# Kernel optimization log

Hardware: AMD Instinct MI355X
Metric: run time of the kernel (lower is better)

Reference implementation:

```python
import jax, jax.numpy as jnp
import numpy as np

N_NODES = 10000
N_EDGES = 160000
N_GRAPHS = 64
F = 80        # hidden dim
T = 5         # towers
F_OUT = 16    # per-tower post output (80/5)
N_LAYERS = 4
EPS = 1e-6
BN_EPS = 1e-5
STD_EPS = 1e-5


def setup_inputs() -> dict:
    key = jax.random.key(0)
    ks = jax.random.split(key, 12)
    x = jax.random.uniform(ks[0], (N_NODES, 2), dtype=jnp.float32)
    edge_index = jax.random.randint(ks[1], (2, N_EDGES), 0, N_NODES, dtype=jnp.int64)
    batch = jnp.sort(jax.random.randint(ks[2], (N_NODES,), 0, N_GRAPHS, dtype=jnp.int64))

    def w(k, shape, fan_in):
        return (jax.random.normal(k, shape, jnp.float32) / np.float32(np.sqrt(fan_in)))

    return {
        "x": x, "edge_index": edge_index, "batch": batch,
        "pre_lin_W": w(ks[3], (1, F), 1), "pre_lin_b": jnp.zeros((F,), jnp.float32),
        "pre_W": w(ks[4], (N_LAYERS, T, 2 * F, F), 2 * F), "pre_b": jnp.zeros((N_LAYERS, T, F), jnp.float32),
        "post_W": w(ks[5], (N_LAYERS, T, 13 * F, F_OUT), 13 * F), "post_b": jnp.zeros((N_LAYERS, T, F_OUT), jnp.float32),
        "lin_W": w(ks[6], (N_LAYERS, F, F), F), "lin_b": jnp.zeros((N_LAYERS, F), jnp.float32),
        "bn_gamma": jnp.ones((N_LAYERS, F), jnp.float32), "bn_beta": jnp.zeros((N_LAYERS, F), jnp.float32),
        "mlp_lin_W": w(ks[7], (40, 1), 40), "mlp_lin_b": jnp.zeros((1,), jnp.float32),
        "mlp1_W": w(ks[8], (40, 20), 40), "mlp1_b": jnp.zeros((20,), jnp.float32),
        "mlp2_W": w(ks[9], (20, 1), 20), "mlp2_b": jnp.zeros((1,), jnp.float32),
    }


def _pna_conv(h, src, dst, deg, avg_log_deg, preW, preb, postW, postb, linW, linb):
    # h: [N, F]; messages per tower: pre MLP over cat(x_i, x_j)  (divide_input=False)
    N = h.shape[0]
    hm = jnp.concatenate([h[dst], h[src]], axis=-1)            # [E, 2F]
    m = jnp.einsum('ef,tfo->eto', hm, preW) + preb             # [E, T, F]

    cnt = jnp.maximum(deg, 1.0)[:, None, None]                 # [N,1,1]
    has = (deg > 0)[:, None, None]
    s = jax.ops.segment_sum(m, dst, num_segments=N)
    mean = s / cnt
    mean_sq = jax.ops.segment_sum(m * m, dst, num_segments=N) / cnt
    mn = jax.ops.segment_min(m, dst, num_segments=N)
    mx = jax.ops.segment_max(m, dst, num_segments=N)
    mn = jnp.where(has, mn, 0.0)
    mx = jnp.where(has, mx, 0.0)
    std = jnp.sqrt(jax.nn.relu(mean_sq - mean * mean) + STD_EPS)
    agg = jnp.concatenate([mean, mn, mx, std], axis=-1)        # [N, T, 4F]

    logd = jnp.log(jnp.maximum(deg, 1.0) + 1.0)[:, None, None]
    amp = agg * (logd / avg_log_deg)
    att = agg * (avg_log_deg / logd)
    out = jnp.concatenate([agg, amp, att], axis=-1)            # [N, T, 12F]

    xt = jnp.broadcast_to(h[:, None, :], (N, T, F))
    out = jnp.concatenate([xt, out], axis=-1)                  # [N, T, 13F]
    out = jnp.einsum('ntf,tfo->nto', out, postW) + postb       # [N, T, F_OUT]
    out = out.reshape(N, T * F_OUT)                            # [N, 80]
    return out @ linW + linb


def _forward(x, edge_index, batch, pre_lin_W, pre_lin_b, pre_W, pre_b,
             post_W, post_b, lin_W, lin_b, bn_gamma, bn_beta,
             mlp_lin_W, mlp_lin_b, mlp1_W, mlp1_b, mlp2_W, mlp2_b):
    N = x.shape[0]
    src, dst = edge_index[0], edge_index[1]
    deg = jax.ops.segment_sum(jnp.ones_like(dst, jnp.float32), dst, num_segments=N)
    avg_log_deg = jnp.mean(jnp.log(deg + 1.0))                 # PNA avg log-degree from deg histogram

    operation = x[:, 0:1]
    assignment = x[:, 1:2]
    op = operation @ pre_lin_W + pre_lin_b                     # [N, 80]

    for l in range(N_LAYERS):
        y = _pna_conv(op, src, dst, deg, avg_log_deg,
                      pre_W[l], pre_b[l], post_W[l], post_b[l], lin_W[l], lin_b[l])
        mu = jnp.mean(y, axis=0)
        var = jnp.mean((y - mu) ** 2, axis=0)                  # biased, training-mode BN
        y = (y - mu) / jnp.sqrt(var + BN_EPS) * bn_gamma[l] + bn_beta[l]
        op = jax.nn.relu(y)

    front, behind = op[:, :40], op[:, 40:]
    xc = front * assignment + behind                           # [N, 40], non-negative

    # LastLayer: log-space scatter-add message passing
    log_score = jax.ops.segment_sum(jnp.log(xc[src] + EPS), dst, num_segments=N)
    xc = jnp.exp(log_score + jnp.log(xc + EPS))

    # global mean pool over graphs
    gcnt = jnp.maximum(jax.ops.segment_sum(jnp.ones_like(batch, jnp.float32), batch, num_segments=N_GRAPHS), 1.0)
    pooled = jax.ops.segment_sum(xc, batch, num_segments=N_GRAPHS) / gcnt[:, None]  # [B, 40]

    x_lin = pooled @ mlp_lin_W + mlp_lin_b
    x_cv = pooled @ mlp1_W + mlp1_b
    x_cv = 20.0 - jax.nn.relu(x_cv)
    x_cv = x_cv @ mlp2_W + mlp2_b
    return x_cv + x_lin                                        # [B, 1]


def reference(x, edge_index, batch, pre_lin_W, pre_lin_b, pre_W, pre_b,
              post_W, post_b, lin_W, lin_b, bn_gamma, bn_beta,
              mlp_lin_W, mlp_lin_b, mlp1_W, mlp1_b, mlp2_W, mlp2_b):
    return _forward(x, edge_index, batch, pre_lin_W, pre_lin_b, pre_W, pre_b,
                    post_W, post_b, lin_W, lin_b, bn_gamma, bn_beta,
                    mlp_lin_W, mlp_lin_b, mlp1_W, mlp1_b, mlp2_W, mlp2_b)
```

## Files before the change

kernel.cpp:

```cpp
#include <hip/hip_runtime.h>
#include <math.h>

#define NN 10000
#define NE 160000
#define NG 64
#define FEAT 80
#define NT 5
#define NL 4

__global__ void k_count(const int* __restrict__ dst, int* __restrict__ deg) {
    int e = blockIdx.x * 256 + threadIdx.x;
    if (e < NE) atomicAdd(&deg[dst[e]], 1);
}

__global__ void k_gcnt(const int* __restrict__ batch, int* __restrict__ gcnt) {
    int n = blockIdx.x * 256 + threadIdx.x;
    if (n < NN) atomicAdd(&gcnt[batch[n]], 1);
}

__global__ void k_scan(const int* __restrict__ deg, int* __restrict__ offs) {
    __shared__ int sums[256];
    int tid = threadIdx.x;
    int start = tid * 40, stop = min(start + 40, NN);
    int s = 0;
    for (int i = start; i < stop; ++i) s += deg[i];
    sums[tid] = s;
    __syncthreads();
    for (int off = 1; off < 256; off <<= 1) {
        int v = (tid >= off) ? sums[tid - off] : 0;
        __syncthreads();
        sums[tid] += v;
        __syncthreads();
    }
    int base = (tid == 0) ? 0 : sums[tid - 1];
    for (int i = start; i < stop; ++i) { offs[i] = base; base += deg[i]; }
    if (tid == 255) offs[NN] = sums[255];
}

__global__ void k_ald(const int* __restrict__ deg, float* __restrict__ ald) {
    __shared__ float red[256];
    int i = blockIdx.x * 256 + threadIdx.x;
    red[threadIdx.x] = (i < NN) ? logf((float)deg[i] + 1.0f) : 0.0f;
    __syncthreads();
    for (int s = 128; s > 0; s >>= 1) {
        if (threadIdx.x < s) red[threadIdx.x] += red[threadIdx.x + s];
        __syncthreads();
    }
    if (threadIdx.x == 0) atomicAdd(ald, red[0]);
}

__global__ void k_fill(const int* __restrict__ src, const int* __restrict__ dst,
                       const int* __restrict__ offs, int* __restrict__ cursor,
                       int* __restrict__ csr) {
    int e = blockIdx.x * 256 + threadIdx.x;
    if (e < NE) {
        int d = dst[e];
        int p = atomicAdd(&cursor[d], 1);
        csr[offs[d] + p] = src[e];
    }
}

__global__ void k_op0(const float* __restrict__ x, const float* __restrict__ plW,
                      const float* __restrict__ plb, float* __restrict__ hT) {
    int i = blockIdx.x * 256 + threadIdx.x;
    if (i < FEAT * NN) {
        int f = i / NN, n = i - f * NN;
        hT[i] = x[2 * n] * plW[f] + plb[f];
    }
}

__global__ __launch_bounds__(256) void k_mm_ab(
        const float* __restrict__ hT, const float* __restrict__ preW_l,
        float* __restrict__ A, float* __restrict__ Bt) {
    __shared__ float hs[16][80];
    int n0 = blockIdx.x * 16;
    int tid = threadIdx.x;
    for (int i = tid; i < 16 * 80; i += 256) {
        int nl = i & 15, f = i >> 4;
        hs[nl][f] = hT[(size_t)f * NN + n0 + nl];
    }
    __syncthreads();
    int c0 = blockIdx.y * 512 + tid;
    float acc[2][16];
#pragma unroll
    for (int s = 0; s < 2; s++)
#pragma unroll
        for (int i = 0; i < 16; i++) acc[s][i] = 0.f;
    const float* wp[2];
#pragma unroll
    for (int s = 0; s < 2; s++) {
        int c = c0 + s * 256;
        int part = (c >= 400) ? 1 : 0;
        int cc = c - part * 400;
        int t = cc / 80, o = cc - t * 80;
        wp[s] = preW_l + (size_t)(t * 160 + part * 80) * 80 + o;
    }
    bool act1 = (c0 + 256) < 800;
    for (int fq = 0; fq < 80; fq += 4) {
        float w0a = wp[0][(fq + 0) * 80], w0b = wp[0][(fq + 1) * 80];
        float w0c = wp[0][(fq + 2) * 80], w0d = wp[0][(fq + 3) * 80];
        float w1a = 0.f, w1b = 0.f, w1c = 0.f, w1d = 0.f;
        if (act1) {
            w1a = wp[1][(fq + 0) * 80]; w1b = wp[1][(fq + 1) * 80];
            w1c = wp[1][(fq + 2) * 80]; w1d = wp[1][(fq + 3) * 80];
        }
#pragma unroll
        for (int i = 0; i < 16; i++) {
            float4 hv = *(const float4*)&hs[i][fq];
            acc[0][i] += hv.x * w0a + hv.y * w0b + hv.z * w0c + hv.w * w0d;
            acc[1][i] += hv.x * w1a + hv.y * w1b + hv.z * w1c + hv.w * w1d;
        }
    }
#pragma unroll
    for (int s = 0; s < 2; s++) {
        int c = c0 + s * 256;
        if (c < 800) {
            int part = (c >= 400) ? 1 : 0;
            int cc = c - part * 400;
            int t = cc / 80, o = cc - t * 80;
            if (part == 0) {
#pragma unroll
                for (int i = 0; i < 16; i++) A[(size_t)(n0 + i) * 400 + cc] = acc[s][i];
            } else {
#pragma unroll
                for (int i = 0; i < 16; i++)
                    Bt[((size_t)t * NN + n0 + i) * 80 + o] = acc[s][i];
            }
        }
    }
}

__global__ __launch_bounds__(256) void k_agg_t(
        const float* __restrict__ A, const float* __restrict__ Bt,
        const int* __restrict__ offs, const int* __restrict__ csr,
        const float* __restrict__ preb_l, float* __restrict__ aggT) {
    __shared__ float st[320 * 17];
    int tid = threadIdx.x;
    int t = blockIdx.y;
    int n0 = blockIdx.x * 16;
    int ni = tid >> 4;
    int cl = tid & 15;
    int n = n0 + ni;
    int e0 = offs[n], e1 = offs[n + 1];
    const float* Bts = Bt + (size_t)t * NN * 80;
    float s[5], q[5], mn[5], mx[5];
#pragma unroll
    for (int k = 0; k < 5; k++) { s[k] = 0.f; q[k] = 0.f; mn[k] = 3.4e38f; mx[k] = -3.4e38f; }
    int e = e0;
    for (; e + 3 < e1; e += 4) {
        const float* br0 = Bts + (size_t)csr[e] * 80 + cl;
        const float* br1 = Bts + (size_t)csr[e + 1] * 80 + cl;
        const float* br2 = Bts + (size_t)csr[e + 2] * 80 + cl;
        const float* br3 = Bts + (size_t)csr[e + 3] * 80 + cl;
#pragma unroll
        for (int k = 0; k < 5; k++) {
            float b0 = br0[k * 16];
            float b1 = br1[k * 16];
            float b2 = br2[k * 16];
            float b3 = br3[k * 16];
            s[k] += (b0 + b1) + (b2 + b3);
            q[k] += (b0 * b0 + b1 * b1) + (b2 * b2 + b3 * b3);
            mn[k] = fminf(mn[k], fminf(fminf(b0, b1), fminf(b2, b3)));
            mx[k] = fmaxf(mx[k], fmaxf(fmaxf(b0, b1), fmaxf(b2, b3)));
        }
    }
    for (; e < e1; ++e) {
        const float* br = Bts + (size_t)csr[e] * 80 + cl;
#pragma unroll
        for (int k = 0; k < 5; k++) {
            float b = br[k * 16];
            s[k] += b; q[k] += b * b;
            mn[k] = fminf(mn[k], b); mx[k] = fmaxf(mx[k], b);
        }
    }
    int d = e1 - e0;
    float degf = (float)d;
    float cnt = fmaxf(degf, 1.f);
#pragma unroll
    for (int k = 0; k < 5; k++) {
        int c = cl + k * 16;
        float a = A[(size_t)n * 400 + t * 80 + c] + preb_l[t * 80 + c];
        float mean = (degf * a + s[k]) / cnt;
        float msq  = (degf * a * a + 2.f * a * s[k] + q[k]) / cnt;
        float sd = sqrtf(fmaxf(msq - mean * mean, 0.f) + 1e-5f);
        float mnr = (d > 0) ? a + mn[k] : 0.f;
        float mxr = (d > 0) ? a + mx[k] : 0.f;
        st[(0 * 80 + c) * 17 + ni] = mean;
        st[(1 * 80 + c) * 17 + ni] = mnr;
        st[(2 * 80 + c) * 17 + ni] = mxr;
        st[(3 * 80 + c) * 17 + ni] = sd;
    }
    __syncthreads();
    int jj = tid >> 4;
    int nl = tid & 15;
#pragma unroll
    for (int pass = 0; pass < 20; ++pass) {
        int j = pass * 16 + jj;
        aggT[((size_t)t * 320 + j) * NN + n0 + nl] = st[j * 17 + nl];
    }
}

__global__ __launch_bounds__(256) void k_post(
        const float* __restrict__ hT, const float* __restrict__ aggT,
        const float* __restrict__ postW_l, const float* __restrict__ postb_l,
        const int* __restrict__ offs, const float* __restrict__ ald_sum,
        float* __restrict__ y0T) {
    __shared__ float wj[80 * 48];
    __shared__ float wh[80 * 16];
    int tid = threadIdx.x;
    int t = blockIdx.y;
    int jq = blockIdx.z;
    int j0 = jq * 80;
    const float* W0 = postW_l + (size_t)t * 1040 * 16;
    const float* W1 = W0 + 80 * 16;
    const float* W2 = W0 + 400 * 16;
    const float* W3 = W0 + 720 * 16;
    for (int idx = tid; idx < 80 * 48; idx += 256) {
        int j = idx / 48;
        int rem = idx - j * 48;
        int p = rem >> 4, o = rem & 15;
        const float* Wp = (p == 0) ? W1 : (p == 1) ? W2 : W3;
        wj[idx] = Wp[(j0 + j) * 16 + o];
    }
    if (jq == 0) {
        for (int idx = tid; idx < 80 * 16; idx += 256)
            wh[idx] = W0[idx];
    }
    __syncthreads();
    int n = blockIdx.x * 256 + tid;
    bool alive = (n < NN);
    int nc = alive ? n : 0;
    float acc1[16], acc2[16], acc3[16];
#pragma unroll
    for (int i = 0; i < 16; i++) { acc1[i] = 0.f; acc2[i] = 0.f; acc3[i] = 0.f; }
    const float* ap = aggT + ((size_t)t * 320 + j0) * NN + nc;
#pragma unroll 8
    for (int j = 0; j < 80; ++j) {
        float a = ap[(size_t)j * NN];
        const float* w = wj + j * 48;
#pragma unroll
        for (int i = 0; i < 16; i++) {
            acc1[i] += a * w[i];
            acc2[i] += a * w[16 + i];
            acc3[i] += a * w[32 + i];
        }
    }
    if (jq == 0) {
#pragma unroll 4
        for (int f = 0; f < 80; ++f) {
            float hv = hT[(size_t)f * NN + nc];
            const float* w = wh + f * 16;
#pragma unroll
            for (int i = 0; i < 16; i++) acc1[i] += hv * w[i];
        }
    }
    if (alive) {
        float degf = (float)(offs[n + 1] - offs[n]);
        float ald = ald_sum[0] * (1.f / NN);
        float logd = logf(fmaxf(degf, 1.f) + 1.f);
        float c1 = logd / ald;
        float c2 = ald / logd;
#pragma unroll
        for (int i = 0; i < 16; i++) {
            float v = acc1[i] + c1 * acc2[i] + c2 * acc3[i];
            if (jq == 0) v += postb_l[t * 16 + i];
            unsafeAtomicAdd(&y0T[(size_t)(t * 16 + i) * NN + n], v);
        }
    }
}

__global__ __launch_bounds__(256) void k_lin(
        const float* __restrict__ y0T, const float* __restrict__ linW_l,
        const float* __restrict__ linb_l, float* __restrict__ yT) {
    __shared__ float ws[80 * 8];
    int tid = threadIdx.x;
    int f0 = blockIdx.y * 8;
    for (int idx = tid; idx < 80 * 8; idx += 256)
        ws[idx] = linW_l[(idx >> 3) * 80 + f0 + (idx & 7)];
    __syncthreads();
    int n = blockIdx.x * 256 + tid;
    bool alive = (n < NN);
    int nc = alive ? n : 0;
    float acc[8];
#pragma unroll
    for (int i = 0; i < 8; i++) acc[i] = 0.f;
#pragma unroll 8
    for (int k = 0; k < 80; ++k) {
        float v = y0T[(size_t)k * NN + nc];
        const float4 wa = *(const float4*)(ws + k * 8);
        const float4 wb = *(const float4*)(ws + k * 8 + 4);
        acc[0] += v * wa.x; acc[1] += v * wa.y; acc[2] += v * wa.z; acc[3] += v * wa.w;
        acc[4] += v * wb.x; acc[5] += v * wb.y; acc[6] += v * wb.z; acc[7] += v * wb.w;
    }
    if (alive) {
#pragma unroll
        for (int i = 0; i < 8; i++)
            yT[(size_t)(f0 + i) * NN + n] = acc[i] + linb_l[f0 + i];
    }
}

__global__ void k_bnstats(const float* __restrict__ yT, float* __restrict__ bnst) {
    __shared__ float r1[256], r2[256];
    int f = blockIdx.x;
    int tid = threadIdx.x;
    float s = 0.f, q = 0.f;
    for (int i = tid; i < NN; i += 256) {
        float v = yT[(size_t)f * NN + i];
        s += v; q += v * v;
    }
    r1[tid] = s; r2[tid] = q;
    __syncthreads();
    for (int st = 128; st > 0; st >>= 1) {
        if (tid < st) { r1[tid] += r1[tid + st]; r2[tid] += r2[tid + st]; }
        __syncthreads();
    }
    if (tid == 0) { bnst[f] = r1[0]; bnst[80 + f] = r2[0]; }
}

__global__ void k_bn(const float* __restrict__ yT, const float* __restrict__ bnst,
                     const float* __restrict__ gamma_l, const float* __restrict__ beta_l,
                     float* __restrict__ hT) {
    int i = blockIdx.x * 256 + threadIdx.x;
    if (i >= FEAT * NN) return;
    int f = i / NN;
    float mu = bnst[f] * (1.f / NN);
    float msq = bnst[80 + f] * (1.f / NN);
    float var = fmaxf(msq - mu * mu, 0.f);
    float v = (yT[i] - mu) * (1.f / sqrtf(var + 1e-5f)) * gamma_l[f] + beta_l[f];
    hT[i] = fmaxf(v, 0.f);
}

__global__ void k_xc(const float* __restrict__ hT, const float* __restrict__ x,
                     float* __restrict__ lxc) {
    int i = blockIdx.x * 256 + threadIdx.x;
    if (i >= 40 * NN) return;
    int j = i / NN, n = i - j * NN;
    float v = hT[(size_t)j * NN + n] * x[2 * n + 1] + hT[(size_t)(40 + j) * NN + n];
    lxc[(size_t)n * 40 + j] = logf(v + 1e-6f);
}

__global__ void k_logagg(const float* __restrict__ lxc, const int* __restrict__ offs,
                         const int* __restrict__ csr, const int* __restrict__ batch,
                         float* __restrict__ pooled) {
    int n = blockIdx.x;
    int tid = threadIdx.x;
    if (tid >= 40) return;
    int e0 = offs[n], e1 = offs[n + 1];
    float s = 0.f;
    for (int k = e0; k < e1; ++k) s += lxc[(size_t)csr[k] * 40 + tid];
    float v = expf(s + lxc[(size_t)n * 40 + tid]);
    atomicAdd(&pooled[batch[n] * 40 + tid], v);
}

__global__ void k_final(const float* __restrict__ pooled, const int* __restrict__ gcnt,
                        const float* __restrict__ mlW, const float* __restrict__ mlb,
                        const float* __restrict__ m1W, const float* __restrict__ m1b,
                        const float* __restrict__ m2W, const float* __restrict__ m2b,
                        float* __restrict__ out) {
    int g = threadIdx.x;
    if (g >= NG) return;
    float inv = 1.f / fmaxf((float)gcnt[g], 1.f);
    float pl[40];
#pragma unroll
    for (int j = 0; j < 40; j++) pl[j] = pooled[g * 40 + j] * inv;
    float xl = mlb[0];
#pragma unroll
    for (int j = 0; j < 40; j++) xl += pl[j] * mlW[j];
    float acc = m2b[0];
    for (int k = 0; k < 20; k++) {
        float v = m1b[k];
#pragma unroll
        for (int j = 0; j < 40; j++) v += pl[j] * m1W[j * 20 + k];
        v = 20.f - fmaxf(v, 0.f);
        acc += v * m2W[k];
    }
    out[g] = acc + xl;
}

extern "C" void kernel_launch(void* const* d_in, const int* in_sizes, int n_in,
                              void* d_out, int out_size, void* d_ws, size_t ws_size,
                              hipStream_t stream) {
    const float* x     = (const float*)d_in[0];
    const int*   ei    = (const int*)d_in[1];
    const int*   batch = (const int*)d_in[2];
    const float* plW   = (const float*)d_in[3];
    const float* plb   = (const float*)d_in[4];
    const float* preW  = (const float*)d_in[5];
    const float* preb  = (const float*)d_in[6];
    const float* postW = (const float*)d_in[7];
    const float* postb = (const float*)d_in[8];
    const float* linW  = (const float*)d_in[9];
    const float* linb  = (const float*)d_in[10];
    const float* bnG   = (const float*)d_in[11];
    const float* bnB   = (const float*)d_in[12];
    const float* mlW   = (const float*)d_in[13];
    const float* mlb   = (const float*)d_in[14];
    const float* m1W   = (const float*)d_in[15];
    const float* m1b   = (const float*)d_in[16];
    const float* m2W   = (const float*)d_in[17];
    const float* m2b   = (const float*)d_in[18];
    float* out = (float*)d_out;
    const int* srcp = ei;
    const int* dstp = ei + NE;

    char* p = (char*)d_ws;
    int*   deg    = (int*)(p + 0);
    int*   cursor = (int*)(p + 40000);
    int*   gcnt   = (int*)(p + 80000);
    float* ald    = (float*)(p + 80256);
    float* pooled = (float*)(p + 80272);
    float* bnst   = (float*)(p + 90512);
    int*   offs   = (int*)(p + 93072);
    int*   csr    = (int*)(p + 133088);
    float* hT     = (float*)(p + 773088);
    float* A      = (float*)(p + 3973088);
    float* Bt     = (float*)(p + 19973088);
    float* aggT   = (float*)(p + 35973088);
    float* y0T = (float*)(p + 23173088);
    float* yT  = (float*)(p + 26373088);
    float* lxc = (float*)(p + 35973088);

    hipMemsetAsync(d_ws, 0, 90512, stream);
    k_count<<<dim3((NE + 255) / 256), 256, 0, stream>>>(dstp, deg);
    k_gcnt<<<dim3((NN + 255) / 256), 256, 0, stream>>>(batch, gcnt);
    k_scan<<<1, 256, 0, stream>>>(deg, offs);
    k_ald<<<dim3((NN + 255) / 256), 256, 0, stream>>>(deg, ald);
    k_fill<<<dim3((NE + 255) / 256), 256, 0, stream>>>(srcp, dstp, offs, cursor, csr);
    k_op0<<<dim3((FEAT * NN + 255) / 256), 256, 0, stream>>>(x, plW, plb, hT);

    for (int l = 0; l < NL; ++l) {
        const float* preW_l  = preW  + (size_t)l * NT * 160 * 80;
        const float* preb_l  = preb  + l * NT * 80;
        const float* postW_l = postW + (size_t)l * NT * 1040 * 16;
        const float* postb_l = postb + l * NT * 16;
        const float* linW_l  = linW  + l * 80 * 80;
        const float* linb_l  = linb  + l * 80;
        float* bnst_l = bnst + l * 160;
        k_mm_ab<<<dim3(625, 2), 256, 0, stream>>>(hT, preW_l, A, Bt);
        k_agg_t<<<dim3(625, 5), 256, 0, stream>>>(A, Bt, offs, csr, preb_l, aggT);
        hipMemsetAsync(y0T, 0, (size_t)80 * NN * 4, stream);
        k_post<<<dim3(40, 5, 4), 256, 0, stream>>>(hT, aggT, postW_l, postb_l, offs, ald, y0T);
        k_lin<<<dim3(40, 10), 256, 0, stream>>>(y0T, linW_l, linb_l, yT);
        k_bnstats<<<dim3(80), 256, 0, stream>>>(yT, bnst_l);
        k_bn<<<dim3((FEAT * NN + 255) / 256), 256, 0, stream>>>(yT, bnst_l, bnG + l * 80, bnB + l * 80, hT);
    }

    k_xc<<<dim3((40 * NN + 255) / 256), 256, 0, stream>>>(hT, x, lxc);
    k_logagg<<<dim3(NN), 64, 0, stream>>>(lxc, offs, csr, batch, pooled);
    k_final<<<1, 64, 0, stream>>>(pooled, gcnt, mlW, mlb, m1W, m1b, m2W, m2b, out);
}
```

Measured before the change: 864.1 us.

## Renumber nodes sorted by descending degree for balanced CSR aggregation

Adds a degree histogram, counting sort and permutation so nodes are renumbered in descending-degree order, and builds the CSR, features, assignment and batch arrays in that permuted order. Adjacent aggregation blocks then handle nodes of similar degree, which should cut load imbalance and wave divergence in the per-node gather kernels. The cost is several extra small setup kernels and an indirect gather in the initial projection. Permutation buffers alias scratch regions (aggT, cursor, deg) that are reused later, which relies on those regions being dead at that point.

```diff
diff --git a/kernel.cpp b/kernel.cpp
--- a/kernel.cpp
+++ b/kernel.cpp
@@ -18,6 +18,55 @@
     if (n < NN) atomicAdd(&gcnt[batch[n]], 1);
 }
 
+__global__ void k_ald(const int* __restrict__ deg, float* __restrict__ ald) {
+    __shared__ float red[256];
+    int i = blockIdx.x * 256 + threadIdx.x;
+    red[threadIdx.x] = (i < NN) ? logf((float)deg[i] + 1.0f) : 0.0f;
+    __syncthreads();
+    for (int s = 128; s > 0; s >>= 1) {
+        if (threadIdx.x < s) red[threadIdx.x] += red[threadIdx.x + s];
+        __syncthreads();
+    }
+    if (threadIdx.x == 0) atomicAdd(ald, red[0]);
+}
+
+__global__ void k_histscan(const int* __restrict__ deg, int* __restrict__ histbase,
+                           int* __restrict__ histcur) {
+    __shared__ int h[256];
+    int tid = threadIdx.x;
+    h[tid] = 0;
+    __syncthreads();
+    for (int i = tid; i < NN; i += 256) {
+        int d = min(deg[i], 255);
+        atomicAdd(&h[d], 1);
+    }
+    __syncthreads();
+    if (tid == 0) {
+        int acc = 0;
+        for (int d = 255; d >= 0; --d) { histbase[d] = acc; acc += h[d]; }
+    }
+    histcur[tid] = 0;
+}
+
+__global__ void k_scatter(const int* __restrict__ deg, const int* __restrict__ histbase,
+                          int* __restrict__ histcur, int* __restrict__ perm,
+                          int* __restrict__ invperm) {
+    int n = blockIdx.x * 256 + threadIdx.x;
+    if (n < NN) {
+        int d = min(deg[n], 255);
+        int p = atomicAdd(&histcur[d], 1);
+        int pn = histbase[d] + p;
+        perm[n] = pn;
+        invperm[pn] = n;
+    }
+}
+
+__global__ void k_degp(const int* __restrict__ deg, const int* __restrict__ invperm,
+                       int* __restrict__ degP) {
+    int pn = blockIdx.x * 256 + threadIdx.x;
+    if (pn < NN) degP[pn] = deg[invperm[pn]];
+}
+
 __global__ void k_scan(const int* __restrict__ deg, int* __restrict__ offs) {
     __shared__ int sums[256];
     int tid = threadIdx.x;
@@ -37,35 +86,35 @@
     if (tid == 255) offs[NN] = sums[255];
 }
 
-__global__ void k_ald(const int* __restrict__ deg, float* __restrict__ ald) {
-    __shared__ float red[256];
-    int i = blockIdx.x * 256 + threadIdx.x;
-    red[threadIdx.x] = (i < NN) ? logf((float)deg[i] + 1.0f) : 0.0f;
-    __syncthreads();
-    for (int s = 128; s > 0; s >>= 1) {
-        if (threadIdx.x < s) red[threadIdx.x] += red[threadIdx.x + s];
-        __syncthreads();
-    }
-    if (threadIdx.x == 0) atomicAdd(ald, red[0]);
-}
-
 __global__ void k_fill(const int* __restrict__ src, const int* __restrict__ dst,
-                       const int* __restrict__ offs, int* __restrict__ cursor,
-                       int* __restrict__ csr) {
+                       const int* __restrict__ perm, const int* __restrict__ offs,
+                       int* __restrict__ cursor, int* __restrict__ csr) {
     int e = blockIdx.x * 256 + threadIdx.x;
     if (e < NE) {
-        int d = dst[e];
-        int p = atomicAdd(&cursor[d], 1);
-        csr[offs[d] + p] = src[e];
-    }
-}
-
-__global__ void k_op0(const float* __restrict__ x, const float* __restrict__ plW,
-                      const float* __restrict__ plb, float* __restrict__ hT) {
+        int pd = perm[dst[e]];
+        int p = atomicAdd(&cursor[pd], 1);
+        csr[offs[pd] + p] = perm[src[e]];
+    }
+}
+
+__global__ void k_prep(const int* __restrict__ invperm, const float* __restrict__ x,
+                       const int* __restrict__ batch, float* __restrict__ asgP,
+                       int* __restrict__ batP) {
+    int pn = blockIdx.x * 256 + threadIdx.x;
+    if (pn < NN) {
+        int n = invperm[pn];
+        asgP[pn] = x[2 * n + 1];
+        batP[pn] = (int)batch[n];
+    }
+}
+
+__global__ void k_op0(const float* __restrict__ x, const int* __restrict__ invperm,
+                      const float* __restrict__ plW, const float* __restrict__ plb,
+                      float* __restrict__ hT) {
     int i = blockIdx.x * 256 + threadIdx.x;
     if (i < FEAT * NN) {
-        int f = i / NN, n = i - f * NN;
-        hT[i] = x[2 * n] * plW[f] + plb[f];
+        int f = i / NN, pn = i - f * NN;
+        hT[i] = x[2 * invperm[pn]] * plW[f] + plb[f];
     }
 }
 
@@ -330,17 +379,17 @@
     hT[i] = fmaxf(v, 0.f);
 }
 
-__global__ void k_xc(const float* __restrict__ hT, const float* __restrict__ x,
+__global__ void k_xc(const float* __restrict__ hT, const float* __restrict__ asgP,
                      float* __restrict__ lxc) {
     int i = blockIdx.x * 256 + threadIdx.x;
     if (i >= 40 * NN) return;
-    int j = i / NN, n = i - j * NN;
-    float v = hT[(size_t)j * NN + n] * x[2 * n + 1] + hT[(size_t)(40 + j) * NN + n];
-    lxc[(size_t)n * 40 + j] = logf(v + 1e-6f);
+    int j = i / NN, pn = i - j * NN;
+    float v = hT[(size_t)j * NN + pn] * asgP[pn] + hT[(size_t)(40 + j) * NN + pn];
+    lxc[(size_t)pn * 40 + j] = logf(v + 1e-6f);
 }
 
 __global__ void k_logagg(const float* __restrict__ lxc, const int* __restrict__ offs,
-                         const int* __restrict__ csr, const int* __restrict__ batch,
+                         const int* __restrict__ csr, const int* __restrict__ batP,
                          float* __restrict__ pooled) {
     int n = blockIdx.x;
     int tid = threadIdx.x;
@@ -349,7 +398,7 @@
     float s = 0.f;
     for (int k = e0; k < e1; ++k) s += lxc[(size_t)csr[k] * 40 + tid];
     float v = expf(s + lxc[(size_t)n * 40 + tid]);
-    atomicAdd(&pooled[batch[n] * 40 + tid], v);
+    atomicAdd(&pooled[batP[n] * 40 + tid], v);
 }
 
 __global__ void k_final(const float* __restrict__ pooled, const int* __restrict__ gcnt,
@@ -419,14 +468,25 @@
     float* y0T = (float*)(p + 23173088);
     float* yT  = (float*)(p + 26373088);
     float* lxc = (float*)(p + 35973088);
+    int* perm     = (int*)((char*)aggT + 0);
+    int* degP     = (int*)((char*)aggT + 40000);
+    int* histbase = (int*)((char*)aggT + 80000);
+    int* histcur  = (int*)((char*)aggT + 81024);
+    int* invperm  = (int*)((char*)aggT + 82048);
+    float* asgP = (float*)cursor;
+    int*   batP = deg;
 
     hipMemsetAsync(d_ws, 0, 90512, stream);
     k_count<<<dim3((NE + 255) / 256), 256, 0, stream>>>(dstp, deg);
     k_gcnt<<<dim3((NN + 255) / 256), 256, 0, stream>>>(batch, gcnt);
-    k_scan<<<1, 256, 0, stream>>>(deg, offs);
     k_ald<<<dim3((NN + 255) / 256), 256, 0, stream>>>(deg, ald);
-    k_fill<<<dim3((NE + 255) / 256), 256, 0, stream>>>(srcp, dstp, offs, cursor, csr);
-    k_op0<<<dim3((FEAT * NN + 255) / 256), 256, 0, stream>>>(x, plW, plb, hT);
+    k_histscan<<<1, 256, 0, stream>>>(deg, histbase, histcur);
+    k_scatter<<<dim3((NN + 255) / 256), 256, 0, stream>>>(deg, histbase, histcur, perm, invperm);
+    k_degp<<<dim3((NN + 255) / 256), 256, 0, stream>>>(deg, invperm, degP);
+    k_scan<<<1, 256, 0, stream>>>(degP, offs);
+    k_fill<<<dim3((NE + 255) / 256), 256, 0, stream>>>(srcp, dstp, perm, offs, cursor, csr);
+    k_prep<<<dim3((NN + 255) / 256), 256, 0, stream>>>(invperm, x, batch, asgP, batP);
+    k_op0<<<dim3((FEAT * NN + 255) / 256), 256, 0, stream>>>(x, invperm, plW, plb, hT);
 
     for (int l = 0; l < NL; ++l) {
         const float* preW_l  = preW  + (size_t)l * NT * 160 * 80;
@@ -445,7 +505,7 @@
         k_bn<<<dim3((FEAT * NN + 255) / 256), 256, 0, stream>>>(yT, bnst_l, bnG + l * 80, bnB + l * 80, hT);
     }
 
-    k_xc<<<dim3((40 * NN + 255) / 256), 256, 0, stream>>>(hT, x, lxc);
-    k_logagg<<<dim3(NN), 64, 0, stream>>>(lxc, offs, csr, batch, pooled);
+    k_xc<<<dim3((40 * NN + 255) / 256), 256, 0, stream>>>(hT, asgP, lxc);
+    k_logagg<<<dim3(NN), 64, 0, stream>>>(lxc, offs, csr, batP, pooled);
     k_final<<<1, 64, 0, stream>>>(pooled, gcnt, mlW, mlb, m1W, m1b, m2W, m2b, out);
 }
```

Measured after the change: 901.4 us. 4.3% more time.
